# Performance work log

Hardware: AMD Instinct MI355X
Metric: run time of the kernel (lower is better)

Reference implementation:

```python
import math
import jax, jax.numpy as jnp
import numpy as np

B, T, C, H = 4, 2048, 1024, 16
D = C // H  # head dim = 64


def setup_inputs() -> dict:
    key = jax.random.key(0)
    ks = jax.random.split(key, 5)
    s = 1.0 / math.sqrt(C)
    return {
        "x": jax.random.normal(ks[0], (B, T, C), jnp.float32),
        "w_qkv": jax.random.normal(ks[1], (C, 3 * C), jnp.float32) * s,
        "b_qkv": jax.random.normal(ks[2], (3 * C,), jnp.float32) * 0.02,
        "w_out": jax.random.normal(ks[3], (C, C), jnp.float32) * s,
        "b_out": jax.random.normal(ks[4], (C,), jnp.float32) * 0.02,
    }


def reference(x, w_qkv, b_qkv, w_out, b_out):
    # qkv projection: (B,T,C) @ (C,3C) -> split into Q,K,V
    qkv = x @ w_qkv + b_qkv
    q, k, v = jnp.split(qkv, 3, axis=-1)
    # reshape to (B,H,T,D)
    q = q.reshape(B, T, H, D).transpose(0, 2, 1, 3)
    k = k.reshape(B, T, H, D).transpose(0, 2, 1, 3)
    v = v.reshape(B, T, H, D).transpose(0, 2, 1, 3)
    # scaled scores with causal mask
    scores = jnp.einsum("bhqd,bhkd->bhqk", q, k) * (1.0 / math.sqrt(D))
    causal = jnp.tril(jnp.ones((T, T), dtype=bool))
    scores = jnp.where(causal[None, None], scores, -jnp.inf)
    attn = jax.nn.softmax(scores, axis=-1)  # dropout_rate=0 (eval)
    out = jnp.einsum("bhqk,bhkd->bhqd", attn, v)
    out = out.transpose(0, 2, 1, 3).reshape(B, T, C)
    return out @ w_out + b_out
```

## Files before the change

### kernel.cpp

```cpp
#include <hip/hip_runtime.h>
#include <cstdint>
#include <cstddef>

typedef _Float16 h8_t __attribute__((ext_vector_type(8)));
typedef _Float16 h4_t __attribute__((ext_vector_type(4)));
typedef float f32x4 __attribute__((ext_vector_type(4)));
typedef float f32x16 __attribute__((ext_vector_type(16)));
typedef unsigned u32x4 __attribute__((ext_vector_type(4)));

#define MFMA_16x16x32_F16(a, b, c) __builtin_amdgcn_mfma_f32_16x16x32_f16(a, b, c, 0, 0, 0)
#define MFMA_32x32x16_F16(a, b, c) __builtin_amdgcn_mfma_f32_32x32x16_f16(a, b, c, 0, 0, 0)

__device__ inline void gload_lds16(const void* g, void* l) {
  __builtin_amdgcn_global_load_lds((const __attribute__((address_space(1))) void*)g,
                                   (__attribute__((address_space(3))) void*)l, 16, 0, 0);
}

#define CFENCE asm volatile("" ::: "memory")
#define RAW_BAR() do { CFENCE; __builtin_amdgcn_s_barrier(); CFENCE; } while (0)

__global__ void cvt_f16_kernel(const float* __restrict__ in, _Float16* __restrict__ out, int n4) {
  int i = blockIdx.x * 256 + threadIdx.x;
  if (i >= n4) return;
  float4 v = reinterpret_cast<const float4*>(in)[i];
  h4_t h;
  h[0] = (_Float16)v.x; h[1] = (_Float16)v.y; h[2] = (_Float16)v.z; h[3] = (_Float16)v.w;
  reinterpret_cast<h4_t*>(out)[i] = h;
}

__global__ void transpose_cvt_kernel(const float* __restrict__ in, _Float16* __restrict__ out,
                                     int R, int Cc) {
  __shared__ float tile[32][33];
  int tx = threadIdx.x & 31;
  int ty = threadIdx.x >> 5;
  int c0 = blockIdx.x * 32;
  int r0 = blockIdx.y * 32;
#pragma unroll
  for (int i = 0; i < 4; ++i)
    tile[ty + i * 8][tx] = in[(size_t)(r0 + ty + i * 8) * Cc + (c0 + tx)];
  __syncthreads();
#pragma unroll
  for (int i = 0; i < 4; ++i)
    out[(size_t)(c0 + ty + i * 8) * R + (r0 + tx)] = (_Float16)tile[tx][ty + i * 8];
}

__global__ __launch_bounds__(512, 2) void gemm_qkv_kernel(
    const _Float16* __restrict__ A, const _Float16* __restrict__ Bt,
    const float* __restrict__ bias, _Float16* __restrict__ outQ,
    _Float16* __restrict__ outK, _Float16* __restrict__ outV) {
  __shared__ _Float16 Al[3][8192];
  __shared__ _Float16 Bl[3][12288];

  const int tid = threadIdx.x;
  const int lane = tid & 63;
  const int w = tid >> 6;
  const int wm = w >> 2, wn = w & 3;
  const int bm = blockIdx.x >> 3;
  const int bn = blockIdx.x & 7;
  const int m0 = bm * 256;
  const int n0 = bn * 384;

  f32x4 acc[8][6];
#pragma unroll
  for (int i = 0; i < 8; ++i)
#pragma unroll
    for (int j = 0; j < 6; ++j) acc[i][j] = (f32x4){0.f, 0.f, 0.f, 0.f};

  const int fg0 = tid >> 6;
  const int sl = tid & 63;
  const int srow = fg0 * 16 + (sl & 15);
  const int scol = (sl >> 4) * 8;
  const _Float16* aS = A + (size_t)(m0 + srow) * 1024 + scol;
  const _Float16* bS = Bt + (size_t)(n0 + srow) * 1024 + scol;
  const int sdst = tid * 8;

  auto stageA = [&](int buf, int kt) {
    const int k0 = kt * 32;
    gload_lds16(aS + k0, &Al[buf][sdst]);
    gload_lds16(aS + 131072 + k0, &Al[buf][sdst + 4096]);
  };
  auto stageB = [&](int buf, int kt) {
    const int k0 = kt * 32;
    gload_lds16(bS + k0, &Bl[buf][sdst]);
    gload_lds16(bS + 131072 + k0, &Bl[buf][sdst + 4096]);
    gload_lds16(bS + 262144 + k0, &Bl[buf][sdst + 8192]);
  };

  const int offA0 = (wm * 8 * 64 + lane) * 8;
  const int offB0 = (wn * 6 * 64 + lane) * 8;

  stageA(0, 0); stageB(0, 0);
  stageA(1, 1); stageB(1, 1);
  asm volatile("s_waitcnt vmcnt(5)" ::: "memory");
  RAW_BAR();

  int cur = 0;
#pragma unroll 1
  for (int t = 0; t < 32; ++t) {
    int nb = cur + 2; if (nb >= 3) nb -= 3;
    const bool st = (t + 2) < 32;
    const _Float16* Ab = &Al[cur][0];
    const _Float16* Bb = &Bl[cur][0];
    h8_t af[4], bf[6];

#pragma unroll
    for (int mf = 0; mf < 4; ++mf) af[mf] = *(const h8_t*)&Ab[offA0 + mf * 512];
#pragma unroll
    for (int nf = 0; nf < 6; ++nf) bf[nf] = *(const h8_t*)&Bb[offB0 + nf * 512];
    if (st) stageA(nb, t + 2);
    RAW_BAR();
    asm volatile("s_waitcnt lgkmcnt(0)" ::: "memory");
    __builtin_amdgcn_sched_barrier(0);
    __builtin_amdgcn_s_setprio(1);
#pragma unroll
    for (int mf = 0; mf < 4; ++mf)
#pragma unroll
      for (int nf = 0; nf < 6; ++nf)
        acc[mf][nf] = MFMA_16x16x32_F16(af[mf], bf[nf], acc[mf][nf]);
    __builtin_amdgcn_s_setprio(0);
    RAW_BAR();

#pragma unroll
    for (int mf = 0; mf < 4; ++mf) af[mf] = *(const h8_t*)&Ab[offA0 + (4 + mf) * 512];
    if (st) stageB(nb, t + 2);
    RAW_BAR();
    asm volatile("s_waitcnt lgkmcnt(0)" ::: "memory");
    __builtin_amdgcn_sched_barrier(0);
    __builtin_amdgcn_s_setprio(1);
#pragma unroll
    for (int mf = 0; mf < 4; ++mf)
#pragma unroll
      for (int nf = 0; nf < 6; ++nf)
        acc[4 + mf][nf] = MFMA_16x16x32_F16(af[mf], bf[nf], acc[4 + mf][nf]);
    __builtin_amdgcn_s_setprio(0);
    if (t < 31) {
      if (st) asm volatile("s_waitcnt vmcnt(5)" ::: "memory");
      else asm volatile("s_waitcnt vmcnt(0)" ::: "memory");
      RAW_BAR();
    }
    ++cur; if (cur == 3) cur = 0;
  }

  const int gm0 = m0 + wm * 128;
  const int gn0 = n0 + wn * 96;
#pragma unroll
  for (int mf = 0; mf < 8; ++mf) {
#pragma unroll
    for (int nf = 0; nf < 6; ++nf) {
      const int gn = gn0 + nf * 16 + (lane & 15);
      const int tm0 = gm0 + mf * 16 + (lane >> 4) * 4;
      const float bv = bias[gn];
      const int which = gn >> 10;
      const int nn = gn & 1023;
      const int h = nn >> 6, d = nn & 63;
      const int t0 = tm0 & 2047, b = tm0 >> 11;
      const int bh = b * 16 + h;
      if (which == 2) {
        h4_t pack;
#pragma unroll
        for (int r = 0; r < 4; ++r) pack[r] = (_Float16)(acc[mf][nf][r] + bv);
        *reinterpret_cast<h4_t*>(&outV[((size_t)bh * 64 + d) * 2048 + t0]) = pack;
      } else {
        _Float16* dst = (which == 0) ? outQ : outK;
        const float scale = (which == 0) ? 0.18033688011112042f : 1.0f;
#pragma unroll
        for (int r = 0; r < 4; ++r)
          dst[((size_t)bh * 2048 + t0 + r) * 64 + d] = (_Float16)((acc[mf][nf][r] + bv) * scale);
      }
    }
  }
}

__global__ __launch_bounds__(256, 3) void gemm_out_kernel(
    const _Float16* __restrict__ A, const _Float16* __restrict__ Bt,
    const float* __restrict__ bias, float* __restrict__ outF, int NB) {
  __shared__ _Float16 Al[3][4096];
  __shared__ _Float16 Bl[3][4096];
  const int tid = threadIdx.x;
  const int lane = tid & 63;
  const int w = tid >> 6;
  const int bm = blockIdx.x / NB;
  const int bn = blockIdx.x % NB;
  const int wm = w & 1, wn = w >> 1;
  const int m0 = bm * 128, n0 = bn * 128;

  f32x4 acc[4][4];
#pragma unroll
  for (int m = 0; m < 4; ++m)
#pragma unroll
    for (int n = 0; n < 4; ++n) acc[m][n] = (f32x4){0.f, 0.f, 0.f, 0.f};

  const int seg0 = w * 2, seg1 = w * 2 + 1;
  const int r0s = seg0 * 16 + (lane >> 2);
  const int r1s = seg1 * 16 + (lane >> 2);
  const int c0s = ((lane & 3) ^ ((r0s >> 1) & 3)) * 8;
  const int c1s = ((lane & 3) ^ ((r1s >> 1) & 3)) * 8;
  const _Float16* aS0 = A + (size_t)(m0 + r0s) * 1024 + c0s;
  const _Float16* aS1 = A + (size_t)(m0 + r1s) * 1024 + c1s;
  const _Float16* bS0 = Bt + (size_t)(n0 + r0s) * 1024 + c0s;
  const _Float16* bS1 = Bt + (size_t)(n0 + r1s) * 1024 + c1s;
  const int d0 = seg0 * 512 + lane * 8;
  const int d1 = seg1 * 512 + lane * 8;

  auto stage = [&](int buf, int kt) {
    const int k0 = kt * 32;
    gload_lds16(aS0 + k0, &Al[buf][d0]);
    gload_lds16(bS0 + k0, &Bl[buf][d0]);
    gload_lds16(aS1 + k0, &Al[buf][d1]);
    gload_lds16(bS1 + k0, &Bl[buf][d1]);
  };

  int offA[4], offB[4];
#pragma unroll
  for (int i = 0; i < 4; ++i) {
    const int rowA = wm * 64 + i * 16 + (lane & 15);
    offA[i] = rowA * 32 + (((lane >> 4) ^ ((rowA >> 1) & 3)) * 8);
    const int rowB = wn * 64 + i * 16 + (lane & 15);
    offB[i] = rowB * 32 + (((lane >> 4) ^ ((rowB >> 1) & 3)) * 8);
  }

  stage(0, 0);
  stage(1, 1);
  asm volatile("s_waitcnt vmcnt(4)" ::: "memory");
  RAW_BAR();

  int cur = 0;
#pragma unroll 1
  for (int t = 0; t < 32; ++t) {
    int nb = cur + 2; if (nb >= 3) nb -= 3;
    if (t + 2 < 32) stage(nb, t + 2);
    const _Float16* Ab = &Al[cur][0];
    const _Float16* Bb = &Bl[cur][0];
    h8_t af[4], bf[4];
#pragma unroll
    for (int i = 0; i < 4; ++i) af[i] = *(const h8_t*)&Ab[offA[i]];
#pragma unroll
    for (int j = 0; j < 4; ++j) bf[j] = *(const h8_t*)&Bb[offB[j]];
#pragma unroll
    for (int i = 0; i < 4; ++i)
#pragma unroll
      for (int j = 0; j < 4; ++j)
        acc[i][j] = MFMA_16x16x32_F16(af[i], bf[j], acc[i][j]);
    if (t < 31) {
      if (t + 2 < 32) asm volatile("s_waitcnt vmcnt(4)" ::: "memory");
      else asm volatile("s_waitcnt vmcnt(0)" ::: "memory");
      RAW_BAR();
    }
    ++cur; if (cur == 3) cur = 0;
  }

  const int gm0 = bm * 128 + wm * 64;
  const int gn0 = bn * 128 + wn * 64;
#pragma unroll
  for (int i = 0; i < 4; ++i) {
#pragma unroll
    for (int j = 0; j < 4; ++j) {
      const int gn = gn0 + j * 16 + (lane & 15);
      const int tm0 = gm0 + i * 16 + (lane >> 4) * 4;
      const float bv = bias[gn];
#pragma unroll
      for (int r = 0; r < 4; ++r)
        outF[(size_t)(tm0 + r) * 1024 + gn] = acc[i][j][r] + bv;
    }
  }
}

__device__ inline void stage_kv(const _Float16* __restrict__ Kbh, const _Float16* __restrict__ Vbh,
                                int kt, _Float16* Kd, _Float16* Vd, int w, int lane) {
  const _Float16* Kg = Kbh + (size_t)kt * 64 * 64;
  const _Float16* Vg = Vbh + kt * 64;
#pragma unroll
  for (int c = 0; c < 2; ++c) {
    const int idx = (2 * w + c) * 64 + lane;
    const int row = idx >> 3;
    const int chs = (idx & 7) ^ (row & 7);
    gload_lds16(Kg + row * 64 + chs * 8, Kd + idx * 8);
    gload_lds16(Vg + (size_t)row * 2048 + chs * 8, Vd + idx * 8);
  }
}

__device__ inline void pack_pfrag(const float* e, h8_t* out) {
  unsigned u[8];
#pragma unroll
  for (int i = 0; i < 8; ++i) {
    auto hv = __builtin_amdgcn_cvt_pkrtz(e[2 * i], e[2 * i + 1]);
    u[i] = __builtin_bit_cast(unsigned, hv);
  }
  auto r02 = __builtin_amdgcn_permlane32_swap(u[0], u[2], false, false);
  auto r13 = __builtin_amdgcn_permlane32_swap(u[1], u[3], false, false);
  auto r46 = __builtin_amdgcn_permlane32_swap(u[4], u[6], false, false);
  auto r57 = __builtin_amdgcn_permlane32_swap(u[5], u[7], false, false);
  u32x4 w0 = {(unsigned)r02[0], (unsigned)r13[0], (unsigned)r02[1], (unsigned)r13[1]};
  u32x4 w1 = {(unsigned)r46[0], (unsigned)r57[0], (unsigned)r46[1], (unsigned)r57[1]};
  out[0] = __builtin_bit_cast(h8_t, w0);
  out[1] = __builtin_bit_cast(h8_t, w1);
}

__global__ __launch_bounds__(256, 2) void attn_kernel(
    const _Float16* __restrict__ Q, const _Float16* __restrict__ K,
    const _Float16* __restrict__ Vt, _Float16* __restrict__ O) {
  __shared__ _Float16 Kl[2][64 * 64];
  __shared__ _Float16 Vl[2][64 * 64];
  const int tid = threadIdx.x;
  const int lane = tid & 63;
  const int w = tid >> 6;
  const int hi = lane >> 5;
  const int l31 = lane & 31;
  const int bh = blockIdx.x >> 3;
  const int pr = blockIdx.x & 7;
  const int b = bh >> 4, h = bh & 15;
  const _Float16* Kbh = K + (size_t)bh * 2048 * 64;
  const _Float16* Vbh = Vt + (size_t)bh * 64 * 2048;

#pragma unroll
  for (int gi = 0; gi < 2; ++gi) {
    const int g = gi ? (15 - pr) : pr;
    const int nt = 2 * g + 2;
    const int qbase = g * 128 + w * 32;
    const int qrow = qbase + l31;

    h8_t qf[4];
    const _Float16* Qp = Q + ((size_t)bh * 2048 + qrow) * 64 + hi * 8;
#pragma unroll
    for (int ds = 0; ds < 4; ++ds)
      qf[ds] = *reinterpret_cast<const h8_t*>(Qp + ds * 16);

    f32x16 oa[2] = {};
    float m = -1e30f, lsum = 0.f;

    stage_kv(Kbh, Vbh, 0, &Kl[0][0], &Vl[0][0], w, lane);
    __syncthreads();

    for (int kt = 0; kt < nt; ++kt) {
      const int cur = kt & 1;
      if (kt + 1 < nt)
        stage_kv(Kbh, Vbh, kt + 1, &Kl[cur ^ 1][0], &Vl[cur ^ 1][0], w, lane);

      if (kt * 64 <= qbase + 31) {
        const char* Kb = (const char*)&Kl[cur][0];
        const char* Vb = (const char*)&Vl[cur][0];
        f32x16 s0 = {}, s1 = {};
#pragma unroll
        for (int ds = 0; ds < 4; ++ds) {
          const int bc = ds * 32 + hi * 16;
          h8_t kf0 = *(const h8_t*)(Kb + l31 * 128 + (bc ^ ((l31 & 7) << 4)));
          h8_t kf1 = *(const h8_t*)(Kb + (32 + l31) * 128 + (bc ^ ((l31 & 7) << 4)));
          s0 = MFMA_32x32x16_F16(kf0, qf[ds], s0);
          s1 = MFMA_32x32x16_F16(kf1, qf[ds], s1);
        }
        if (kt >= 2 * g) {
#pragma unroll
          for (int r = 0; r < 16; ++r) {
            const int kr = kt * 64 + (r & 3) + 8 * (r >> 2) + 4 * hi;
            if (kr > qrow) s0[r] = -1e30f;
            if (kr + 32 > qrow) s1[r] = -1e30f;
          }
        }
        float t[16];
#pragma unroll
        for (int r = 0; r < 16; ++r) t[r] = fmaxf(s0[r], s1[r]);
#pragma unroll
        for (int st = 8; st >= 1; st >>= 1)
#pragma unroll
          for (int r = 0; r < st; ++r) t[r] = fmaxf(t[r], t[r + st]);
        const float pmax = fmaxf(t[0], __shfl_xor(t[0], 32));
        const float mnew = fmaxf(m, pmax);
        if (__any(mnew > m + 8.f)) {
          const float al = __builtin_amdgcn_exp2f(m - mnew);
          lsum *= al;
#pragma unroll
          for (int r = 0; r < 16; ++r) { oa[0][r] *= al; oa[1][r] *= al; }
          m = mnew;
        }
        float e0[16], e1[16];
#pragma unroll
        for (int r = 0; r < 16; ++r) {
          e0[r] = __builtin_amdgcn_exp2f(s0[r] - m);
          e1[r] = __builtin_amdgcn_exp2f(s1[r] - m);
        }
        float ps = 0.f;
#pragma unroll
        for (int r = 0; r < 16; ++r) ps += e0[r] + e1[r];
        ps += __shfl_xor(ps, 32);
        lsum += ps;
        h8_t pf[4];
        pack_pfrag(e0, pf + 0);
        pack_pfrag(e1, pf + 2);
#pragma unroll
        for (int dt = 0; dt < 2; ++dt) {
#pragma unroll
          for (int kg = 0; kg < 4; ++kg) {
            const int row = dt * 32 + l31;
            const int bc = kg * 32 + hi * 16;
            h8_t vf = *(const h8_t*)(Vb + row * 128 + (bc ^ ((row & 7) << 4)));
            oa[dt] = MFMA_32x32x16_F16(vf, pf[kg], oa[dt]);
          }
        }
      }
      __syncthreads();
    }

    const float inv = __builtin_amdgcn_rcpf(lsum);
    _Float16* Op = O + ((size_t)b * 2048 + qrow) * 1024 + h * 64;
#pragma unroll
    for (int dt = 0; dt < 2; ++dt) {
#pragma unroll
      for (int rg = 0; rg < 4; ++rg) {
        h4_t pk4;
#pragma unroll
        for (int i = 0; i < 4; ++i) pk4[i] = (_Float16)(oa[dt][rg * 4 + i] * inv);
        *reinterpret_cast<h4_t*>(Op + dt * 32 + rg * 8 + hi * 4) = pk4;
      }
    }
  }
}

extern "C" void kernel_launch(void* const* d_in, const int* in_sizes, int n_in,
                              void* d_out, int out_size, void* d_ws, size_t ws_size,
                              hipStream_t stream) {
  (void)in_sizes; (void)n_in; (void)out_size; (void)ws_size;
  const float* x = (const float*)d_in[0];
  const float* w_qkv = (const float*)d_in[1];
  const float* b_qkv = (const float*)d_in[2];
  const float* w_out = (const float*)d_in[3];
  const float* b_out = (const float*)d_in[4];
  float* out = (float*)d_out;

  char* ws = (char*)d_ws;
  size_t off = 0;
  auto alloc = [&](size_t bytes) {
    void* p = ws + off;
    off += (bytes + 255) & ~(size_t)255;
    return p;
  };
  _Float16* x16 = (_Float16*)alloc((size_t)8192 * 1024 * 2);
  _Float16* wqkvT = (_Float16*)alloc((size_t)3072 * 1024 * 2);
  _Float16* woutT = (_Float16*)alloc((size_t)1024 * 1024 * 2);
  _Float16* Qh = (_Float16*)alloc((size_t)64 * 2048 * 64 * 2);
  _Float16* Kh = (_Float16*)alloc((size_t)64 * 2048 * 64 * 2);
  _Float16* Vth = (_Float16*)alloc((size_t)64 * 64 * 2048 * 2);
  _Float16* Oh = (_Float16*)alloc((size_t)8192 * 1024 * 2);

  cvt_f16_kernel<<<8192, 256, 0, stream>>>(x, x16, 8192 * 1024 / 4);
  transpose_cvt_kernel<<<dim3(3072 / 32, 1024 / 32), 256, 0, stream>>>(w_qkv, wqkvT, 1024, 3072);
  transpose_cvt_kernel<<<dim3(1024 / 32, 1024 / 32), 256, 0, stream>>>(w_out, woutT, 1024, 1024);
  gemm_qkv_kernel<<<256, 512, 0, stream>>>(x16, wqkvT, b_qkv, Qh, Kh, Vth);
  attn_kernel<<<64 * 8, 256, 0, stream>>>(Qh, Kh, Vth, Oh);
  gemm_out_kernel<<<64 * 8, 256, 0, stream>>>(Oh, woutT, b_out, out, 8);
}
```

Measured before the change: 179.1 us.

## Process 128-key tiles per iteration in attention with a double-buffered 2x64 stage

Restructures the attention inner loop to stage and consume two 64-key K/V subtiles per iteration, so there are 128 keys per step. This halves the number of barriers and online-softmax max/rescale passes per row block. It doubles LDS use to 64KB per block, which may limit occupancy at 2 blocks/CU, and it raises register pressure from holding four score accumulators.

After: 177.6 us. Within noise of the previous version (-0.8%).

```diff
diff --git a/kernel.cpp b/kernel.cpp
--- a/kernel.cpp
+++ b/kernel.cpp
@@ -265,8 +265,8 @@
   }
 }
 
-__device__ inline void stage_kv(const _Float16* __restrict__ Kbh, const _Float16* __restrict__ Vbh,
-                                int kt, _Float16* Kd, _Float16* Vd, int w, int lane) {
+__device__ inline void stage_kv64(const _Float16* __restrict__ Kbh, const _Float16* __restrict__ Vbh,
+                                  int kt, _Float16* Kd, _Float16* Vd, int w, int lane) {
   const _Float16* Kg = Kbh + (size_t)kt * 64 * 64;
   const _Float16* Vg = Vbh + kt * 64;
 #pragma unroll
@@ -299,8 +299,8 @@
 __global__ __launch_bounds__(256, 2) void attn_kernel(
     const _Float16* __restrict__ Q, const _Float16* __restrict__ K,
     const _Float16* __restrict__ Vt, _Float16* __restrict__ O) {
-  __shared__ _Float16 Kl[2][64 * 64];
-  __shared__ _Float16 Vl[2][64 * 64];
+  __shared__ _Float16 Kl[2][2][64 * 64];
+  __shared__ _Float16 Vl[2][2][64 * 64];
   const int tid = threadIdx.x;
   const int lane = tid & 63;
   const int w = tid >> 6;
@@ -315,7 +315,7 @@
 #pragma unroll
   for (int gi = 0; gi < 2; ++gi) {
     const int g = gi ? (15 - pr) : pr;
-    const int nt = 2 * g + 2;
+    const int nT = g + 1;
     const int qbase = g * 128 + w * 32;
     const int qrow = qbase + l31;
 
@@ -328,64 +328,93 @@
     f32x16 oa[2] = {};
     float m = -1e30f, lsum = 0.f;
 
-    stage_kv(Kbh, Vbh, 0, &Kl[0][0], &Vl[0][0], w, lane);
+    stage_kv64(Kbh, Vbh, 0, &Kl[0][0][0], &Vl[0][0][0], w, lane);
+    stage_kv64(Kbh, Vbh, 1, &Kl[0][1][0], &Vl[0][1][0], w, lane);
     __syncthreads();
 
-    for (int kt = 0; kt < nt; ++kt) {
-      const int cur = kt & 1;
-      if (kt + 1 < nt)
-        stage_kv(Kbh, Vbh, kt + 1, &Kl[cur ^ 1][0], &Vl[cur ^ 1][0], w, lane);
-
-      if (kt * 64 <= qbase + 31) {
-        const char* Kb = (const char*)&Kl[cur][0];
-        const char* Vb = (const char*)&Vl[cur][0];
-        f32x16 s0 = {}, s1 = {};
-#pragma unroll
-        for (int ds = 0; ds < 4; ++ds) {
-          const int bc = ds * 32 + hi * 16;
-          h8_t kf0 = *(const h8_t*)(Kb + l31 * 128 + (bc ^ ((l31 & 7) << 4)));
-          h8_t kf1 = *(const h8_t*)(Kb + (32 + l31) * 128 + (bc ^ ((l31 & 7) << 4)));
-          s0 = MFMA_32x32x16_F16(kf0, qf[ds], s0);
-          s1 = MFMA_32x32x16_F16(kf1, qf[ds], s1);
+#pragma unroll 1
+    for (int T = 0; T < nT; ++T) {
+      const int cur = T & 1;
+      if (T + 1 < nT) {
+        stage_kv64(Kbh, Vbh, 2 * (T + 1), &Kl[cur ^ 1][0][0], &Vl[cur ^ 1][0][0], w, lane);
+        stage_kv64(Kbh, Vbh, 2 * (T + 1) + 1, &Kl[cur ^ 1][1][0], &Vl[cur ^ 1][1][0], w, lane);
+      }
+
+      const bool diag = (T == g);
+      const bool skip1 = diag && (w < 2);
+      f32x16 s[2][2];
+
+#pragma unroll
+      for (int half = 0; half < 2; ++half) {
+        if (half == 1 && skip1) {
+#pragma unroll
+          for (int r = 0; r < 16; ++r) { s[1][0][r] = -1e30f; s[1][1][r] = -1e30f; }
+        } else {
+          const char* Kb = (const char*)&Kl[cur][half][0];
+          f32x16 a0 = {}, a1 = {};
+#pragma unroll
+          for (int ds = 0; ds < 4; ++ds) {
+            const int bc = ds * 32 + hi * 16;
+            h8_t kf0 = *(const h8_t*)(Kb + l31 * 128 + (bc ^ ((l31 & 7) << 4)));
+            h8_t kf1 = *(const h8_t*)(Kb + (32 + l31) * 128 + (bc ^ ((l31 & 7) << 4)));
+            a0 = MFMA_32x32x16_F16(kf0, qf[ds], a0);
+            a1 = MFMA_32x32x16_F16(kf1, qf[ds], a1);
+          }
+          s[half][0] = a0;
+          s[half][1] = a1;
         }
-        if (kt >= 2 * g) {
+      }
+      if (diag) {
+#pragma unroll
+        for (int half = 0; half < 2; ++half) {
+          if (half == 1 && skip1) continue;
 #pragma unroll
           for (int r = 0; r < 16; ++r) {
-            const int kr = kt * 64 + (r & 3) + 8 * (r >> 2) + 4 * hi;
-            if (kr > qrow) s0[r] = -1e30f;
-            if (kr + 32 > qrow) s1[r] = -1e30f;
+            const int kr = T * 128 + half * 64 + (r & 3) + 8 * (r >> 2) + 4 * hi;
+            if (kr > qrow) s[half][0][r] = -1e30f;
+            if (kr + 32 > qrow) s[half][1][r] = -1e30f;
           }
         }
-        float t[16];
-#pragma unroll
-        for (int r = 0; r < 16; ++r) t[r] = fmaxf(s0[r], s1[r]);
-#pragma unroll
-        for (int st = 8; st >= 1; st >>= 1)
-#pragma unroll
-          for (int r = 0; r < st; ++r) t[r] = fmaxf(t[r], t[r + st]);
-        const float pmax = fmaxf(t[0], __shfl_xor(t[0], 32));
-        const float mnew = fmaxf(m, pmax);
-        if (__any(mnew > m + 8.f)) {
-          const float al = __builtin_amdgcn_exp2f(m - mnew);
-          lsum *= al;
-#pragma unroll
-          for (int r = 0; r < 16; ++r) { oa[0][r] *= al; oa[1][r] *= al; }
-          m = mnew;
-        }
-        float e0[16], e1[16];
-#pragma unroll
-        for (int r = 0; r < 16; ++r) {
-          e0[r] = __builtin_amdgcn_exp2f(s0[r] - m);
-          e1[r] = __builtin_amdgcn_exp2f(s1[r] - m);
-        }
-        float ps = 0.f;
-#pragma unroll
-        for (int r = 0; r < 16; ++r) ps += e0[r] + e1[r];
-        ps += __shfl_xor(ps, 32);
-        lsum += ps;
+      }
+
+      float t[16];
+#pragma unroll
+      for (int r = 0; r < 16; ++r)
+        t[r] = fmaxf(fmaxf(s[0][0][r], s[0][1][r]), fmaxf(s[1][0][r], s[1][1][r]));
+#pragma unroll
+      for (int st = 8; st >= 1; st >>= 1)
+#pragma unroll
+        for (int r = 0; r < st; ++r) t[r] = fmaxf(t[r], t[r + st]);
+      const float pmax = fmaxf(t[0], __shfl_xor(t[0], 32));
+      const float mnew = fmaxf(m, pmax);
+      if (__any(mnew > m + 8.f)) {
+        const float al = __builtin_amdgcn_exp2f(m - mnew);
+        lsum *= al;
+#pragma unroll
+        for (int r = 0; r < 16; ++r) { oa[0][r] *= al; oa[1][r] *= al; }
+        m = mnew;
+      }
+      float ps = 0.f;
+#pragma unroll
+      for (int half = 0; half < 2; ++half)
+#pragma unroll
+        for (int sub = 0; sub < 2; ++sub)
+#pragma unroll
+          for (int r = 0; r < 16; ++r) {
+            const float pv = __builtin_amdgcn_exp2f(s[half][sub][r] - m);
+            s[half][sub][r] = pv;
+            ps += pv;
+          }
+      ps += __shfl_xor(ps, 32);
+      lsum += ps;
+
+#pragma unroll
+      for (int half = 0; half < 2; ++half) {
+        if (half == 1 && skip1) continue;
         h8_t pf[4];
-        pack_pfrag(e0, pf + 0);
-        pack_pfrag(e1, pf + 2);
+        pack_pfrag((const float*)&s[half][0], pf + 0);
+        pack_pfrag((const float*)&s[half][1], pf + 2);
+        const char* Vb = (const char*)&Vl[cur][half][0];
 #pragma unroll
         for (int dt = 0; dt < 2; ++dt) {
 #pragma unroll
```
